# Optimization experiments

Hardware: AMD Instinct MI355X
Metric: run time of the kernel (lower is better)

The kernel has to match this reference:

```python
import jax, jax.numpy as jnp
import numpy as np

B, C, H, W = 8, 512, 64, 64
HEADS, GROUPS, EPS = 4, 32, 1e-5


def setup_inputs() -> dict:
    key = jax.random.key(0)
    ks = jax.random.split(key, 7)
    s = 0.02
    return {
        "x": jax.random.normal(ks[0], (B, C, H, W), dtype=jnp.float32),
        "gn_w": jnp.ones((C,), dtype=jnp.float32),
        "gn_b": jnp.zeros((C,), dtype=jnp.float32),
        "qkv_w": jax.random.normal(ks[1], (3 * C, C), dtype=jnp.float32) * s,
        "qkv_b": jnp.zeros((3 * C,), dtype=jnp.float32),
        "proj_w": jax.random.normal(ks[2], (C, C), dtype=jnp.float32) * s,
        "proj_b": jnp.zeros((C,), dtype=jnp.float32),
    }


def reference(x, gn_w, gn_b, qkv_w, qkv_b, proj_w, proj_b):
    b, c, h, w = x.shape
    d = c // HEADS  # per-head channel dim
    n = h * w
    # GroupNorm(32, C)
    xg = x.reshape(b, GROUPS, -1)
    mu = xg.mean(axis=-1, keepdims=True)
    var = xg.var(axis=-1, keepdims=True)
    hn = ((xg - mu) * jax.lax.rsqrt(var + EPS)).reshape(b, c, h, w)
    hn = hn * gn_w[:, None, None] + gn_b[:, None, None]
    # 1x1 conv qkv: [3C, C] contraction over channels
    qkv = jnp.einsum('oc,bchw->bohw', qkv_w, hn) + qkv_b[:, None, None]
    qkv = qkv.reshape(b, 3, HEADS, d, n)
    q, k, v = qkv[:, 0], qkv[:, 1], qkv[:, 2]  # each [b, heads, d, n]
    # NOTE: as in the source, q @ k^T contracts over spatial dim -> [b,heads,d,d]
    attn = jnp.einsum('bhdn,bhen->bhde', q, k) * (d ** -0.5)
    attn = jax.nn.softmax(attn, axis=-1)
    out = jnp.einsum('bhde,bhen->bhdn', attn, v).reshape(b, c, h, w)
    out = jnp.einsum('oc,bchw->bohw', proj_w, out) + proj_b[:, None, None]
    return x + out
```

## Files before the change

### kernel.cpp

```cpp
#include <hip/hip_runtime.h>
#include <hip/hip_bf16.h>

typedef __hip_bfloat16 bf16;
typedef __bf16 v8bf __attribute__((ext_vector_type(8)));
typedef float  v4f  __attribute__((ext_vector_type(4)));

struct __align__(8) bf16x4 { bf16 x, y, z, w; };

__device__ __forceinline__ bf16 f2b(float v) { return __float2bfloat16(v); }

#define NSP 4096
#define CCH 512

__device__ __forceinline__ void async_cp16(const bf16* g, __bf16* l) {
    __builtin_amdgcn_global_load_lds(
        (const __attribute__((address_space(1))) unsigned int*)(unsigned long long)g,
        (__attribute__((address_space(3))) unsigned int*)(unsigned int)(unsigned long long)l,
        16, 0, 0);
}

__global__ __launch_bounds__(256) void wconv2_kernel(const float* __restrict__ qw,
                                                     const float* __restrict__ pw,
                                                     bf16* __restrict__ qd,
                                                     bf16* __restrict__ pd) {
    int i = blockIdx.x * 256 + threadIdx.x;
    if (i < 196608) {
        float4 v = ((const float4*)qw)[i];
        bf16x4 o = { f2b(v.x), f2b(v.y), f2b(v.z), f2b(v.w) };
        ((bf16x4*)qd)[i] = o;
    } else {
        int j = i - 196608;
        float4 v = ((const float4*)pw)[j];
        bf16x4 o = { f2b(v.x), f2b(v.y), f2b(v.z), f2b(v.w) };
        ((bf16x4*)pd)[j] = o;
    }
}

__global__ __launch_bounds__(1024) void gn_stats_kernel(const float* __restrict__ x,
                                                        float* __restrict__ stats) {
    int blk = blockIdx.x;
    int b = blk >> 5, g = blk & 31;
    size_t base = ((size_t)(b * CCH + g * 16)) * NSP;
    const float4* xp4 = (const float4*)(x + base);
    int t = threadIdx.x;
    float s = 0.f, s2 = 0.f;
    for (int i = t; i < 16384; i += 1024) {
        float4 v = xp4[i];
        s  += v.x + v.y + v.z + v.w;
        s2 += v.x * v.x + v.y * v.y + v.z * v.z + v.w * v.w;
    }
    for (int off = 32; off > 0; off >>= 1) {
        s  += __shfl_down(s, off);
        s2 += __shfl_down(s2, off);
    }
    __shared__ float red[32];
    int wid = t >> 6, lid = t & 63;
    if (lid == 0) { red[wid] = s; red[wid + 16] = s2; }
    __syncthreads();
    if (t == 0) {
        float ts = 0.f, ts2 = 0.f;
#pragma unroll
        for (int w = 0; w < 16; ++w) { ts += red[w]; ts2 += red[w + 16]; }
        float mean = ts * (1.f / 65536.f);
        float var  = ts2 * (1.f / 65536.f) - mean * mean;
        stats[blk * 2]     = mean;
        stats[blk * 2 + 1] = rsqrtf(var + 1e-5f);
    }
}

__global__ __launch_bounds__(256) void gn_norm_t_kernel(const float* __restrict__ x,
                                                        const float* __restrict__ gw,
                                                        const float* __restrict__ gb,
                                                        const float* __restrict__ stats,
                                                        bf16* __restrict__ hnT) {
    __shared__ float sT[64][65];
    int n0 = blockIdx.x * 64, c0 = blockIdx.y * 64, b = blockIdx.z;
    int t = threadIdx.x;
    int cl = t >> 4, nl4 = (t & 15) << 2;
#pragma unroll
    for (int it = 0; it < 4; ++it) {
        int crow = cl + it * 16;
        int c = c0 + crow;
        int bg = b * 32 + (c >> 4);
        float mean = stats[bg * 2], rstd = stats[bg * 2 + 1];
        float wsc = gw[c] * rstd;
        float bb  = gb[c] - mean * wsc;
        float4 v = *(const float4*)&x[((long)b * CCH + c) * NSP + n0 + nl4];
        sT[crow][nl4 + 0] = v.x * wsc + bb;
        sT[crow][nl4 + 1] = v.y * wsc + bb;
        sT[crow][nl4 + 2] = v.z * wsc + bb;
        sT[crow][nl4 + 3] = v.w * wsc + bb;
    }
    __syncthreads();
    int nl = t >> 4, cl4 = (t & 15) << 2;
#pragma unroll
    for (int it = 0; it < 4; ++it) {
        int nrow = nl + it * 16;
        bf16x4 ov = { f2b(sT[cl4 + 0][nrow]), f2b(sT[cl4 + 1][nrow]),
                      f2b(sT[cl4 + 2][nrow]), f2b(sT[cl4 + 3][nrow]) };
        *(bf16x4*)&hnT[((long)b * NSP + n0 + nrow) * CCH + c0 + cl4] = ov;
    }
}

__device__ __forceinline__ void gemm_core(const bf16* __restrict__ A, long as,
                                          const bf16* __restrict__ B, long bs,
                                          int K, v4f acc[4][4],
                                          __bf16* sA, __bf16* sB) {
    int t = threadIdx.x;
    int lane = t & 63, wv = t >> 6;
    int wr = wv >> 1, wc = wv & 1;
    int lq = lane & 15, quad = lane >> 4;
    int r0 = wv * 16 + (lane >> 2);
    int koff = (lane & 3) * 8;
    __bf16* ldsA0 = sA + wv * 512 + lane * 8;
    __bf16* ldsA1 = ldsA0 + 2048;
    __bf16* ldsB0 = sB + wv * 512 + lane * 8;
    __bf16* ldsB1 = ldsB0 + 2048;
    const __bf16* aBase = sA + (wr * 64) * 32;
    const __bf16* bBase = sB + (wc * 64) * 32;

    for (int k0 = 0; k0 < K; k0 += 32) {
        __syncthreads();
        async_cp16(A + (long)r0 * as + k0 + koff,        ldsA0);
        async_cp16(A + (long)(r0 + 64) * as + k0 + koff, ldsA1);
        async_cp16(B + (long)r0 * bs + k0 + koff,        ldsB0);
        async_cp16(B + (long)(r0 + 64) * bs + k0 + koff, ldsB1);
        __syncthreads();
        v8bf a[4], bf[4];
#pragma unroll
        for (int i = 0; i < 4; ++i)
            a[i] = *(const v8bf*)(aBase + (i * 16 + lq) * 32 + quad * 8);
#pragma unroll
        for (int j = 0; j < 4; ++j)
            bf[j] = *(const v8bf*)(bBase + (j * 16 + lq) * 32 + quad * 8);
#pragma unroll
        for (int i = 0; i < 4; ++i)
#pragma unroll
            for (int j = 0; j < 4; ++j)
                acc[i][j] = __builtin_amdgcn_mfma_f32_16x16x32_bf16(a[i], bf[j], acc[i][j], 0, 0, 0);
    }
}

__device__ __forceinline__ void gemm256_core(const bf16* __restrict__ A, long lda,
                                             const bf16* __restrict__ B, long ldb,
                                             int K, v4f acc[8][4], char* sLds) {
    const int t = threadIdx.x;
    const int lane = t & 63, wv = t >> 6;
    const int wm = wv >> 2, wn = wv & 3;
    const int lq = lane & 15, quad = lane >> 4;
    const int xsw = (lq & 7) << 4;
    const int kq0 = ((quad << 4)) ^ xsw;
    const int kq1 = (64 | (quad << 4)) ^ xsw;
    const int aRow0 = (wm * 128 + lq) << 7;
    const int bRow0 = (wn * 64 + lq) << 7;
    const int NT = K >> 6;

    auto STAGE = [&](const bf16* mb, long ld, int ldsbyte, int ktile, int h) {
#pragma unroll
        for (int s = 0; s < 2; ++s) {
            int L = (s << 13) + (t << 4);
            int row = L >> 7;
            int kb = (L & 127) ^ ((row & 7) << 4);
            const char* g = (const char*)(mb + (long)(h * 128 + row) * ld + (long)ktile * 64);
            async_cp16((const bf16*)(g + kb),
                       (__bf16*)(sLds + ldsbyte + (h << 14) + L));
        }
    };

    STAGE(B, ldb, 32768, 0, 0);
    STAGE(B, ldb, 32768, 0, 1);
    STAGE(A, lda, 0,     0, 0);
    STAGE(A, lda, 0,     0, 1);
    if (NT > 1) {
        STAGE(B, ldb, 65536 + 32768, 1, 0);
        STAGE(B, ldb, 65536 + 32768, 1, 1);
        asm volatile("s_waitcnt vmcnt(4)" ::: "memory");
    } else {
        asm volatile("s_waitcnt vmcnt(0)" ::: "memory");
    }
    __builtin_amdgcn_s_barrier();
    asm volatile("" ::: "memory");

    for (int kt = 0; kt < NT; ++kt) {
        const int cb = (kt & 1) << 16;
        const int nb = cb ^ 65536;
        const int bufA = cb, bufB = cb | 32768;
        v8bf a[4][2], b0[2][2], b1[2][2];

#pragma unroll
        for (int ii = 0; ii < 4; ++ii) {
            a[ii][0] = *(const v8bf*)(sLds + bufA + aRow0 + ((ii * 16) << 7) + kq0);
            a[ii][1] = *(const v8bf*)(sLds + bufA + aRow0 + ((ii * 16) << 7) + kq1);
        }
#pragma unroll
        for (int jj = 0; jj < 2; ++jj) {
            b0[jj][0] = *(const v8bf*)(sLds + bufB + bRow0 + ((jj * 16) << 7) + kq0);
            b0[jj][1] = *(const v8bf*)(sLds + bufB + bRow0 + ((jj * 16) << 7) + kq1);
        }
        if (kt + 1 < NT) STAGE(A, lda, nb, kt + 1, 0);
        __builtin_amdgcn_s_setprio(1);
#pragma unroll
        for (int ii = 0; ii < 4; ++ii)
#pragma unroll
            for (int jj = 0; jj < 2; ++jj) {
                acc[ii][jj] = __builtin_amdgcn_mfma_f32_16x16x32_bf16(a[ii][0], b0[jj][0], acc[ii][jj], 0, 0, 0);
                acc[ii][jj] = __builtin_amdgcn_mfma_f32_16x16x32_bf16(a[ii][1], b0[jj][1], acc[ii][jj], 0, 0, 0);
            }
        __builtin_amdgcn_s_setprio(0);
        __builtin_amdgcn_s_barrier();
        asm volatile("" ::: "memory");

#pragma unroll
        for (int jj = 0; jj < 2; ++jj) {
            b1[jj][0] = *(const v8bf*)(sLds + bufB + bRow0 + ((32 + jj * 16) << 7) + kq0);
            b1[jj][1] = *(const v8bf*)(sLds + bufB + bRow0 + ((32 + jj * 16) << 7) + kq1);
        }
        if (kt + 1 < NT) STAGE(A, lda, nb, kt + 1, 1);
        __builtin_amdgcn_s_setprio(1);
#pragma unroll
        for (int ii = 0; ii < 4; ++ii)
#pragma unroll
            for (int jj = 0; jj < 2; ++jj) {
                acc[ii][2 + jj] = __builtin_amdgcn_mfma_f32_16x16x32_bf16(a[ii][0], b1[jj][0], acc[ii][2 + jj], 0, 0, 0);
                acc[ii][2 + jj] = __builtin_amdgcn_mfma_f32_16x16x32_bf16(a[ii][1], b1[jj][1], acc[ii][2 + jj], 0, 0, 0);
            }
        __builtin_amdgcn_s_setprio(0);
        __builtin_amdgcn_s_barrier();
        asm volatile("" ::: "memory");

#pragma unroll
        for (int ii = 0; ii < 4; ++ii) {
            a[ii][0] = *(const v8bf*)(sLds + bufA + aRow0 + ((64 + ii * 16) << 7) + kq0);
            a[ii][1] = *(const v8bf*)(sLds + bufA + aRow0 + ((64 + ii * 16) << 7) + kq1);
        }
        if (kt + 2 < NT) STAGE(B, ldb, bufB, kt + 2, 0);
        __builtin_amdgcn_s_setprio(1);
#pragma unroll
        for (int ii = 0; ii < 4; ++ii)
#pragma unroll
            for (int jj = 0; jj < 2; ++jj) {
                acc[4 + ii][2 + jj] = __builtin_amdgcn_mfma_f32_16x16x32_bf16(a[ii][0], b1[jj][0], acc[4 + ii][2 + jj], 0, 0, 0);
                acc[4 + ii][2 + jj] = __builtin_amdgcn_mfma_f32_16x16x32_bf16(a[ii][1], b1[jj][1], acc[4 + ii][2 + jj], 0, 0, 0);
            }
        __builtin_amdgcn_s_setprio(0);
        __builtin_amdgcn_s_barrier();
        asm volatile("" ::: "memory");

        if (kt + 2 < NT) STAGE(B, ldb, bufB, kt + 2, 1);
        __builtin_amdgcn_s_setprio(1);
#pragma unroll
        for (int ii = 0; ii < 4; ++ii)
#pragma unroll
            for (int jj = 0; jj < 2; ++jj) {
                acc[4 + ii][jj] = __builtin_amdgcn_mfma_f32_16x16x32_bf16(a[ii][0], b0[jj][0], acc[4 + ii][jj], 0, 0, 0);
                acc[4 + ii][jj] = __builtin_amdgcn_mfma_f32_16x16x32_bf16(a[ii][1], b0[jj][1], acc[4 + ii][jj], 0, 0, 0);
            }
        __builtin_amdgcn_s_setprio(0);
        if (kt + 2 < NT) asm volatile("s_waitcnt vmcnt(4)" ::: "memory");
        else             asm volatile("s_waitcnt vmcnt(0)" ::: "memory");
        __builtin_amdgcn_s_barrier();
        asm volatile("" ::: "memory");
    }
}

__global__ __launch_bounds__(512, 2) void qkv_gemm_kernel(const bf16* __restrict__ hnT,
                                                          const bf16* __restrict__ qkv_wb,
                                                          const float* __restrict__ qkv_b,
                                                          bf16* __restrict__ qkbuf,
                                                          bf16* __restrict__ vT) {
    __shared__ __align__(16) char sLds[131072];
    int n0 = blockIdx.x * 256, o0 = blockIdx.y * 256, b = blockIdx.z;
    v4f acc[8][4] = {};
    gemm256_core(hnT + ((long)b * NSP + n0) * CCH, CCH,
                 qkv_wb + (long)o0 * CCH, CCH, CCH, acc, sLds);
    int t = threadIdx.x, lane = t & 63, wv = t >> 6, wm = wv >> 2, wn = wv & 3;
    int lq = lane & 15, quad = lane >> 4;
    if (o0 < 1024) {
#pragma unroll
        for (int j = 0; j < 4; ++j) {
            int o = o0 + wn * 64 + j * 16 + lq;
            float bias = qkv_b[o];
#pragma unroll
            for (int i = 0; i < 8; ++i) {
                int n = n0 + wm * 128 + i * 16 + quad * 4;
                v4f v = acc[i][j];
                bf16x4 ov = { f2b(v[0] + bias), f2b(v[1] + bias),
                              f2b(v[2] + bias), f2b(v[3] + bias) };
                *(bf16x4*)&qkbuf[((long)b * 1024 + o) * NSP + n] = ov;
            }
        }
    } else {
#pragma unroll
        for (int j = 0; j < 4; ++j) {
            int e = o0 - 1024 + wn * 64 + j * 16 + lq;
            float bias = qkv_b[1024 + e];
#pragma unroll
            for (int i = 0; i < 8; ++i) {
                int n = n0 + wm * 128 + i * 16 + quad * 4;
                v4f v = acc[i][j];
#pragma unroll
                for (int r = 0; r < 4; ++r)
                    vT[((long)b * NSP + n + r) * CCH + e] = f2b(v[r] + bias);
            }
        }
    }
}

__global__ __launch_bounds__(256) void qk_gemm_kernel(const bf16* __restrict__ qkbuf,
                                                      float* __restrict__ P_part) {
    __shared__ __align__(16) __bf16 sA[128 * 32];
    __shared__ __align__(16) __bf16 sB[128 * 32];
    int s = blockIdx.x, bh = blockIdx.y;
    int b = bh >> 2, h = bh & 3;
    const bf16* q  = qkbuf + ((long)b * 1024 + h * 128) * NSP + s * 256;
    const bf16* kk = qkbuf + ((long)b * 1024 + 512 + h * 128) * NSP + s * 256;
    v4f acc[4][4] = {};
    gemm_core(q, NSP, kk, NSP, 256, acc, sA, sB);
    float* Pp = P_part + ((long)s * 32 + bh) * 16384;
    int t = threadIdx.x, lane = t & 63, wv = t >> 6, wr = wv >> 1, wc = wv & 1;
    int lq = lane & 15, quad = lane >> 4;
#pragma unroll
    for (int j = 0; j < 4; ++j) {
        int e = wc * 64 + j * 16 + lq;
#pragma unroll
        for (int i = 0; i < 4; ++i) {
            int d = wr * 64 + i * 16 + quad * 4;
            v4f v = acc[i][j];
#pragma unroll
            for (int r = 0; r < 4; ++r) Pp[(long)(d + r) * 128 + e] = v[r];
        }
    }
}

__global__ __launch_bounds__(128) void softmax_kernel(const float* __restrict__ P_part,
                                                      bf16* __restrict__ Pb) {
    int row = blockIdx.x;
    int bh = row >> 7, d = row & 127;
    int t = threadIdx.x;
    float v = 0.f;
#pragma unroll
    for (int s = 0; s < 16; ++s)
        v += P_part[((long)s * 32 + bh) * 16384 + (long)d * 128 + t];
    v *= 0.08838834764831845f;
    float m = v;
    for (int off = 32; off > 0; off >>= 1) m = fmaxf(m, __shfl_down(m, off));
    __shared__ float sm[2];
    if ((t & 63) == 0) sm[t >> 6] = m;
    __syncthreads();
    m = fmaxf(sm[0], sm[1]);
    float e = __expf(v - m);
    float ssum = e;
    for (int off = 32; off > 0; off >>= 1) ssum += __shfl_down(ssum, off);
    __shared__ float ss[2];
    if ((t & 63) == 0) ss[t >> 6] = ssum;
    __syncthreads();
    ssum = ss[0] + ss[1];
    Pb[(long)row * 128 + t] = f2b(e / ssum);
}

__global__ __launch_bounds__(256) void pv_gemm_kernel(const bf16* __restrict__ Pb,
                                                      const bf16* __restrict__ vT,
                                                      bf16* __restrict__ attT) {
    __shared__ __align__(16) __bf16 sA[128 * 32];
    __shared__ __align__(16) __bf16 sB[128 * 32];
    int n0 = blockIdx.x * 128, bh = blockIdx.y;
    int b = bh >> 2, h = bh & 3;
    v4f acc[4][4] = {};
    gemm_core(Pb + (long)bh * 16384, 128,
              vT + ((long)b * NSP + n0) * CCH + h * 128, CCH, 128, acc, sA, sB);
    int t = threadIdx.x, lane = t & 63, wv = t >> 6, wr = wv >> 1, wc = wv & 1;
    int lq = lane & 15, quad = lane >> 4;
#pragma unroll
    for (int j = 0; j < 4; ++j) {
        int n = n0 + wc * 64 + j * 16 + lq;
#pragma unroll
        for (int i = 0; i < 4; ++i) {
            int d = wr * 64 + i * 16 + quad * 4;
            v4f v = acc[i][j];
            bf16x4 ov = { f2b(v[0]), f2b(v[1]), f2b(v[2]), f2b(v[3]) };
            *(bf16x4*)&attT[((long)b * NSP + n) * CCH + h * 128 + d] = ov;
        }
    }
}

__global__ __launch_bounds__(512, 2) void proj_gemm_kernel(const bf16* __restrict__ attT,
                                                           const bf16* __restrict__ proj_wb,
                                                           const float* __restrict__ proj_b,
                                                           const float* __restrict__ x,
                                                           float* __restrict__ out) {
    __shared__ __align__(16) char sLds[131072];
    int n0 = blockIdx.x * 256, c0 = blockIdx.y * 256, b = blockIdx.z;
    v4f acc[8][4] = {};
    gemm256_core(attT + ((long)b * NSP + n0) * CCH, CCH,
                 proj_wb + (long)c0 * CCH, CCH, CCH, acc, sLds);
    int t = threadIdx.x, lane = t & 63, wv = t >> 6, wm = wv >> 2, wn = wv & 3;
    int lq = lane & 15, quad = lane >> 4;
#pragma unroll
    for (int j = 0; j < 4; ++j) {
        int c = c0 + wn * 64 + j * 16 + lq;
        float bias = proj_b[c];
#pragma unroll
        for (int i = 0; i < 8; ++i) {
            int n = n0 + wm * 128 + i * 16 + quad * 4;
            long idx = ((long)b * CCH + c) * NSP + n;
            float4 r = *(const float4*)&x[idx];
            v4f v = acc[i][j];
            float4 ov = { v[0] + bias + r.x, v[1] + bias + r.y,
                          v[2] + bias + r.z, v[3] + bias + r.w };
            *(float4*)&out[idx] = ov;
        }
    }
}

extern "C" void kernel_launch(void* const* d_in, const int* in_sizes, int n_in,
                              void* d_out, int out_size, void* d_ws, size_t ws_size,
                              hipStream_t stream) {
    const float* x      = (const float*)d_in[0];
    const float* gn_w   = (const float*)d_in[1];
    const float* gn_b   = (const float*)d_in[2];
    const float* qkv_w  = (const float*)d_in[3];
    const float* qkv_b  = (const float*)d_in[4];
    const float* proj_w = (const float*)d_in[5];
    const float* proj_b = (const float*)d_in[6];
    float* out = (float*)d_out;

    char* ws = (char*)d_ws;
    bf16*  hnT    = (bf16*)ws;
    float* P_part = (float*)ws;
    bf16*  attT   = (bf16*)ws;
    bf16*  qkbuf  = (bf16*)(ws + 33554432);
    bf16*  vT     = (bf16*)(ws + 100663296);
    bf16*  Pb     = (bf16*)(ws + 134217728);
    float* stats  = (float*)(ws + 135266304);
    bf16*  qkv_wb = (bf16*)(ws + 135270400);
    bf16*  proj_wb= (bf16*)(ws + 136843264);

    wconv2_kernel<<<1024, 256, 0, stream>>>(qkv_w, proj_w, qkv_wb, proj_wb);
    gn_stats_kernel<<<256, 1024, 0, stream>>>(x, stats);
    gn_norm_t_kernel<<<dim3(64, 8, 8), 256, 0, stream>>>(x, gn_w, gn_b, stats, hnT);
    qkv_gemm_kernel<<<dim3(16, 6, 8), 512, 0, stream>>>(hnT, qkv_wb, qkv_b, qkbuf, vT);
    qk_gemm_kernel<<<dim3(16, 32), 256, 0, stream>>>(qkbuf, P_part);
    softmax_kernel<<<4096, 128, 0, stream>>>(P_part, Pb);
    pv_gemm_kernel<<<dim3(32, 32), 256, 0, stream>>>(Pb, vT, attT);
    proj_gemm_kernel<<<dim3(16, 2, 8), 512, 0, stream>>>(attT, proj_wb, proj_b, x, out);
}
```

Before: 283.9 us.

## Fuse weight conversion into GN stats and softmax into QK kernel via counters

Merges the weight fp32-to-bf16 conversion kernel with the GroupNorm statistics kernel into a single prologue launch, which also zeroes per-head counters. The split-K QK^T kernel now bumps an atomic counter per (batch, head) after writing its partial sums. The last block to arrive reduces the 16 partials and applies softmax in place, so the separate softmax launch is gone. This removes two launches, but the softmax now runs serially on only 32 blocks (4 waves each handling 32 rows), and correctness depends on threadfence ordering.

New measurement: 405.5 us. 1.43x slower.

```diff
diff --git a/kernel.cpp b/kernel.cpp
--- a/kernel.cpp
+++ b/kernel.cpp
@@ -19,30 +19,33 @@
         16, 0, 0);
 }
 
-__global__ __launch_bounds__(256) void wconv2_kernel(const float* __restrict__ qw,
-                                                     const float* __restrict__ pw,
-                                                     bf16* __restrict__ qd,
-                                                     bf16* __restrict__ pd) {
-    int i = blockIdx.x * 256 + threadIdx.x;
-    if (i < 196608) {
-        float4 v = ((const float4*)qw)[i];
-        bf16x4 o = { f2b(v.x), f2b(v.y), f2b(v.z), f2b(v.w) };
-        ((bf16x4*)qd)[i] = o;
-    } else {
-        int j = i - 196608;
-        float4 v = ((const float4*)pw)[j];
-        bf16x4 o = { f2b(v.x), f2b(v.y), f2b(v.z), f2b(v.w) };
-        ((bf16x4*)pd)[j] = o;
-    }
-}
-
-__global__ __launch_bounds__(1024) void gn_stats_kernel(const float* __restrict__ x,
-                                                        float* __restrict__ stats) {
+__global__ __launch_bounds__(1024) void prologue_kernel(const float* __restrict__ x,
+                                                        float* __restrict__ stats,
+                                                        const float* __restrict__ qw,
+                                                        const float* __restrict__ pw,
+                                                        bf16* __restrict__ qd,
+                                                        bf16* __restrict__ pd,
+                                                        unsigned* __restrict__ cnt) {
     int blk = blockIdx.x;
+    int t = threadIdx.x;
+    if (blk == 0 && t < 32) cnt[t] = 0u;
+    if (blk >= 256) {
+        int i = (blk - 256) * 1024 + t;
+        if (i < 196608) {
+            float4 v = ((const float4*)qw)[i];
+            bf16x4 o = { f2b(v.x), f2b(v.y), f2b(v.z), f2b(v.w) };
+            ((bf16x4*)qd)[i] = o;
+        } else {
+            int j = i - 196608;
+            float4 v = ((const float4*)pw)[j];
+            bf16x4 o = { f2b(v.x), f2b(v.y), f2b(v.z), f2b(v.w) };
+            ((bf16x4*)pd)[j] = o;
+        }
+        return;
+    }
     int b = blk >> 5, g = blk & 31;
     size_t base = ((size_t)(b * CCH + g * 16)) * NSP;
     const float4* xp4 = (const float4*)(x + base);
-    int t = threadIdx.x;
     float s = 0.f, s2 = 0.f;
     for (int i = t; i < 16384; i += 1024) {
         float4 v = xp4[i];
@@ -307,7 +310,9 @@
 }
 
 __global__ __launch_bounds__(256) void qk_gemm_kernel(const bf16* __restrict__ qkbuf,
-                                                      float* __restrict__ P_part) {
+                                                      float* __restrict__ P_part,
+                                                      bf16* __restrict__ Pb,
+                                                      unsigned* __restrict__ cnt) {
     __shared__ __align__(16) __bf16 sA[128 * 32];
     __shared__ __align__(16) __bf16 sB[128 * 32];
     int s = blockIdx.x, bh = blockIdx.y;
@@ -330,32 +335,33 @@
             for (int r = 0; r < 4; ++r) Pp[(long)(d + r) * 128 + e] = v[r];
         }
     }
-}
-
-__global__ __launch_bounds__(128) void softmax_kernel(const float* __restrict__ P_part,
-                                                      bf16* __restrict__ Pb) {
-    int row = blockIdx.x;
-    int bh = row >> 7, d = row & 127;
-    int t = threadIdx.x;
-    float v = 0.f;
-#pragma unroll
-    for (int s = 0; s < 16; ++s)
-        v += P_part[((long)s * 32 + bh) * 16384 + (long)d * 128 + t];
-    v *= 0.08838834764831845f;
-    float m = v;
-    for (int off = 32; off > 0; off >>= 1) m = fmaxf(m, __shfl_down(m, off));
-    __shared__ float sm[2];
-    if ((t & 63) == 0) sm[t >> 6] = m;
+    __threadfence();
+    __shared__ unsigned oldc;
+    if (t == 0) oldc = atomicAdd(&cnt[bh], 1u);
     __syncthreads();
-    m = fmaxf(sm[0], sm[1]);
-    float e = __expf(v - m);
-    float ssum = e;
-    for (int off = 32; off > 0; off >>= 1) ssum += __shfl_down(ssum, off);
-    __shared__ float ss[2];
-    if ((t & 63) == 0) ss[t >> 6] = ssum;
-    __syncthreads();
-    ssum = ss[0] + ss[1];
-    Pb[(long)row * 128 + t] = f2b(e / ssum);
+    if (oldc == 15u) {
+        __threadfence();
+        for (int d = wv * 32; d < wv * 32 + 32; ++d) {
+            float v0 = 0.f, v1 = 0.f;
+#pragma unroll
+            for (int sp = 0; sp < 16; ++sp) {
+                const float* row = P_part + ((long)sp * 32 + bh) * 16384 + (long)d * 128;
+                v0 += row[lane];
+                v1 += row[lane + 64];
+            }
+            v0 *= 0.08838834764831845f;
+            v1 *= 0.08838834764831845f;
+            float m = fmaxf(v0, v1);
+            for (int off = 32; off > 0; off >>= 1) m = fmaxf(m, __shfl_xor(m, off));
+            float e0 = __expf(v0 - m), e1 = __expf(v1 - m);
+            float ss = e0 + e1;
+            for (int off = 32; off > 0; off >>= 1) ss += __shfl_xor(ss, off);
+            float inv = 1.f / ss;
+            bf16* outr = Pb + (long)bh * 16384 + (long)d * 128;
+            outr[lane]      = f2b(e0 * inv);
+            outr[lane + 64] = f2b(e1 * inv);
+        }
+    }
 }
 
 __global__ __launch_bounds__(256) void pv_gemm_kernel(const bf16* __restrict__ Pb,
@@ -432,15 +438,15 @@
     bf16*  vT     = (bf16*)(ws + 100663296);
     bf16*  Pb     = (bf16*)(ws + 134217728);
     float* stats  = (float*)(ws + 135266304);
+    unsigned* cnt = (unsigned*)(ws + 135268352);
     bf16*  qkv_wb = (bf16*)(ws + 135270400);
     bf16*  proj_wb= (bf16*)(ws + 136843264);
 
-    wconv2_kernel<<<1024, 256, 0, stream>>>(qkv_w, proj_w, qkv_wb, proj_wb);
-    gn_stats_kernel<<<256, 1024, 0, stream>>>(x, stats);
+    prologue_kernel<<<512, 1024, 0, stream>>>(x, stats, qkv_w, proj_w,
+                                              qkv_wb, proj_wb, cnt);
     gn_norm_t_kernel<<<dim3(64, 8, 8), 256, 0, stream>>>(x, gn_w, gn_b, stats, hnT);
     qkv_gemm_kernel<<<dim3(16, 6, 8), 512, 0, stream>>>(hnT, qkv_wb, qkv_b, qkbuf, vT);
-    qk_gemm_kernel<<<dim3(16, 32), 256, 0, stream>>>(qkbuf, P_part);
-    softmax_kernel<<<4096, 128, 0, stream>>>(P_part, Pb);
+    qk_gemm_kernel<<<dim3(16, 32), 256, 0, stream>>>(qkbuf, P_part, Pb, cnt);
     pv_gemm_kernel<<<dim3(32, 32), 256, 0, stream>>>(Pb, vT, attT);
     proj_gemm_kernel<<<dim3(16, 2, 8), 512, 0, stream>>>(attT, proj_wb, proj_b, x, out);
 }
```
